# Performance work log

Measured on AMD Instinct MI355X. Metric: run time of the kernel, lower is better.

## Reference

```python
import jax, jax.numpy as jnp
import numpy as np

EPS = 1e-6
N_HEADS = 16
KV_HEADS = 4
HEAD_DIM = 64
N_REP = N_HEADS // KV_HEADS
N_EXPERTS = 8
TOP_K = 2


def _rms_norm(x, w):
    return x * jax.lax.rsqrt(jnp.mean(x * x, axis=-1, keepdims=True) + EPS) * w


def _apply_rope(x, fc):
    # x: (B,T,H,D); fc: (T, D//2, 2) holding (cos, sin)
    B, T, H, D = x.shape
    xr = x.reshape(B, T, H, D // 2, 2)
    f = fc.reshape(1, T, 1, D // 2, 2)
    re = xr[..., 0] * f[..., 0] - xr[..., 1] * f[..., 1]
    im = xr[..., 1] * f[..., 0] + xr[..., 0] * f[..., 1]
    return jnp.stack([re, im], axis=-1).reshape(B, T, H, D)


def _silu(x):
    return x * jax.nn.sigmoid(x)


def setup_inputs():
    key = jax.random.key(0)
    ks = jax.random.split(key, 16)
    B, T, C = 4, 1024, 1024
    IE, IS = 1024, 2048  # expert_inter_dim, shared inter_dim
    s = 0.02
    x = jax.random.normal(ks[0], (B, T, C), jnp.float32)
    inv_freq = 1.0 / (10000.0 ** (np.arange(0, HEAD_DIM, 2, dtype=np.float32) / HEAD_DIM))
    ang = np.outer(np.arange(T, dtype=np.float32), inv_freq)
    freq_cis = jnp.asarray(np.stack([np.cos(ang), np.sin(ang)], axis=-1), jnp.float32)
    causal = np.tril(np.ones((T, T), dtype=bool))
    mask = jnp.asarray(np.where(causal, 0.0, -1e9), dtype=jnp.float32).reshape(1, 1, T, T)
    window = jnp.zeros((1, 1, T, T), jnp.float32)
    return {
        "x": x,
        "freq_cis": freq_cis,
        "mask": mask,
        "window": window,
        "norm1_w": jnp.ones((C,), jnp.float32),
        "wq": jax.random.normal(ks[1], (N_HEADS * HEAD_DIM, C), jnp.float32) * s,
        "wk": jax.random.normal(ks[2], (KV_HEADS * HEAD_DIM, C), jnp.float32) * s,
        "wv": jax.random.normal(ks[3], (KV_HEADS * HEAD_DIM, C), jnp.float32) * s,
        "wo": jax.random.normal(ks[4], (C, N_HEADS * HEAD_DIM), jnp.float32) * s,
        "norm2_w": jnp.ones((C,), jnp.float32),
        "gate_w": jax.random.normal(ks[5], (N_EXPERTS, C), jnp.float32) * s,
        "exp_w1": jax.random.normal(ks[6], (N_EXPERTS, IE, C), jnp.float32) * s,
        "exp_w2": jax.random.normal(ks[7], (N_EXPERTS, IE, C), jnp.float32) * s,
        "exp_wp": jax.random.normal(ks[8], (N_EXPERTS, C, IE), jnp.float32) * s,
        "sh_w1": jax.random.normal(ks[9], (IS, C), jnp.float32) * s,
        "sh_w2": jax.random.normal(ks[10], (IS, C), jnp.float32) * s,
        "sh_wp": jax.random.normal(ks[11], (C, IS), jnp.float32) * s,
        "start_pos": 0,
    }


def reference(x, freq_cis, mask, window, norm1_w, wq, wk, wv, wo, norm2_w,
              gate_w, exp_w1, exp_w2, exp_wp, sh_w1, sh_w2, sh_wp, start_pos):
    B, T, C = x.shape
    # ---- pre-norm attention (GQA, Global mask, eval: no dropout) ----
    xn = _rms_norm(x, norm1_w)
    q = (xn @ wq.T).reshape(B, T, N_HEADS, HEAD_DIM)
    k = (xn @ wk.T).reshape(B, T, KV_HEADS, HEAD_DIM)
    v = (xn @ wv.T).reshape(B, T, KV_HEADS, HEAD_DIM)
    q = _apply_rope(q, freq_cis)
    k = _apply_rope(k, freq_cis)
    k = jnp.repeat(k, N_REP, axis=2)  # (B,T,H,D)
    v = jnp.repeat(v, N_REP, axis=2)
    scale = 1.0 / np.sqrt(HEAD_DIM).astype(np.float32)
    att = jnp.einsum("bqhd,bkhd->bhqk", q, k) * scale + mask
    p = jax.nn.softmax(att, axis=-1)
    o = jnp.einsum("bhqk,bkhd->bqhd", p, v).reshape(B, T, C)
    x = x + o @ wo.T
    # ---- pre-norm MoE FFN ----
    xn2 = _rms_norm(x, norm2_w).reshape(-1, C)  # (N,C)
    scores = xn2 @ gate_w.T                      # gate logits, returned
    probs = jax.nn.softmax(scores, axis=-1)
    top_w, top_i = jax.lax.top_k(probs, TOP_K)   # (N,K)
    # dense combine weights (N,E): zero for non-selected experts
    wfull = jnp.sum(jax.nn.one_hot(top_i, N_EXPERTS, dtype=x.dtype) * top_w[..., None], axis=1)
    h = _silu(jnp.einsum("nc,eic->eni", xn2, exp_w1)) * jnp.einsum("nc,eic->eni", xn2, exp_w2)
    ye = jnp.einsum("eni,eci->enc", h, exp_wp)   # per-expert outputs
    y = jnp.einsum("ne,enc->nc", wfull, ye)      # routed combine
    z = (_silu(xn2 @ sh_w1.T) * (xn2 @ sh_w2.T)) @ sh_wp.T  # shared expert
    out = x + (y + z).reshape(B, T, C)
    return out, scores
```

## Files before the change

kernel.cpp:

```cpp
#include <hip/hip_runtime.h>


typedef __bf16 bf16_t;
typedef __bf16 bf16x8 __attribute__((ext_vector_type(8)));
typedef __bf16 bf16x4 __attribute__((ext_vector_type(4)));
typedef float  f32x4  __attribute__((ext_vector_type(4)));

#define GLD16(gp, lp) __builtin_amdgcn_global_load_lds(                         \
    (const __attribute__((address_space(1))) void*)(gp),                        \
    (__attribute__((address_space(3))) void*)(lp), 16, 0, 0)

__global__ __launch_bounds__(256) void convert_k(
    const float* __restrict__ src, bf16_t* __restrict__ dst)
{
    size_t i = (size_t)blockIdx.x * 256 + threadIdx.x;
    float4 v = *((const float4*)src + i);
    bf16x4 o;
    o[0] = (bf16_t)v.x; o[1] = (bf16_t)v.y; o[2] = (bf16_t)v.z; o[3] = (bf16_t)v.w;
    *((bf16x4*)dst + i) = o;
}

__global__ __launch_bounds__(256) void gemm_bt(
    const bf16_t* __restrict__ A, const bf16_t* __restrict__ W,
    int M, int N, int K, int ldw, int mode,
    float* __restrict__ outF, bf16_t* __restrict__ outB,
    const float* __restrict__ resF)
{
    __shared__ __align__(16) bf16_t sA[128 * 64];
    __shared__ __align__(16) bf16_t sB[128 * 64];
    const int tid  = threadIdx.x;
    const int bm   = blockIdx.y * 128, bn = blockIdx.x * 128;
    const int lane = tid & 63;
    const int wv   = tid >> 6;
    const int wm   = (wv >> 1) * 64, wn = (wv & 1) * 64;
    const int lr   = lane & 15;
    const int kg   = lane >> 4;

    f32x4 acc[4][4];
    #pragma unroll
    for (int i = 0; i < 4; ++i)
        #pragma unroll
        for (int j = 0; j < 4; ++j)
            acc[i][j] = f32x4{0.f, 0.f, 0.f, 0.f};

    for (int k0 = 0; k0 < K; k0 += 64) {
        #pragma unroll
        for (int p = 0; p < 4; ++p) {
            int idx = p * 256 + tid;
            int row = idx >> 3, ch = (idx & 7) * 8;
            GLD16(A + (size_t)(bm + row) * K   + k0 + ch, sA + idx * 8);
            GLD16(W + (size_t)(bn + row) * ldw + k0 + ch, sB + idx * 8);
        }
        __syncthreads();
        #pragma unroll
        for (int ks = 0; ks < 2; ++ks) {
            bf16x8 af[4], bfr[4];
            #pragma unroll
            for (int i = 0; i < 4; ++i)
                af[i] = *(const bf16x8*)(sA + (wm + i * 16 + lr) * 64 + ks * 32 + kg * 8);
            #pragma unroll
            for (int j = 0; j < 4; ++j)
                bfr[j] = *(const bf16x8*)(sB + (wn + j * 16 + lr) * 64 + ks * 32 + kg * 8);
            #pragma unroll
            for (int i = 0; i < 4; ++i)
                #pragma unroll
                for (int j = 0; j < 4; ++j)
                    acc[i][j] = __builtin_amdgcn_mfma_f32_16x16x32_bf16(
                        af[i], bfr[j], acc[i][j], 0, 0, 0);
        }
        __syncthreads();
    }

    #pragma unroll
    for (int i = 0; i < 4; ++i) {
        #pragma unroll
        for (int j = 0; j < 4; ++j) {
            #pragma unroll
            for (int rr = 0; rr < 4; ++rr) {
                int m = bm + wm + i * 16 + kg * 4 + rr;
                int n = bn + wn + j * 16 + lr;
                size_t o = (size_t)m * N + n;
                float v = acc[i][j][rr];
                if (mode == 0)      outF[o] = v;
                else if (mode == 1) outB[o] = (bf16_t)v;
                else                outF[o] = v + resF[o];
            }
        }
    }
}

__global__ __launch_bounds__(256) void gemm_glu(
    const bf16_t* __restrict__ A, const bf16_t* __restrict__ W1,
    const bf16_t* __restrict__ W2, int M, int N, int K,
    bf16_t* __restrict__ out)
{
    __shared__ __align__(16) bf16_t sA[128 * 64];
    __shared__ __align__(16) bf16_t sB1[128 * 64];
    __shared__ __align__(16) bf16_t sB2[128 * 64];
    const int tid  = threadIdx.x;
    const int bm   = blockIdx.y * 128, bn = blockIdx.x * 128;
    const int lane = tid & 63;
    const int wv   = tid >> 6;
    const int wm   = (wv >> 1) * 64, wn = (wv & 1) * 64;
    const int lr   = lane & 15;
    const int kg   = lane >> 4;

    f32x4 acc1[4][4], acc2[4][4];
    #pragma unroll
    for (int i = 0; i < 4; ++i)
        #pragma unroll
        for (int j = 0; j < 4; ++j) {
            acc1[i][j] = f32x4{0.f, 0.f, 0.f, 0.f};
            acc2[i][j] = f32x4{0.f, 0.f, 0.f, 0.f};
        }

    for (int k0 = 0; k0 < K; k0 += 64) {
        #pragma unroll
        for (int p = 0; p < 4; ++p) {
            int idx = p * 256 + tid;
            int row = idx >> 3, ch = (idx & 7) * 8;
            GLD16(A  + (size_t)(bm + row) * K + k0 + ch, sA  + idx * 8);
            GLD16(W1 + (size_t)(bn + row) * K + k0 + ch, sB1 + idx * 8);
            GLD16(W2 + (size_t)(bn + row) * K + k0 + ch, sB2 + idx * 8);
        }
        __syncthreads();
        #pragma unroll
        for (int ks = 0; ks < 2; ++ks) {
            bf16x8 af[4], b1[4], b2[4];
            #pragma unroll
            for (int i = 0; i < 4; ++i)
                af[i] = *(const bf16x8*)(sA + (wm + i * 16 + lr) * 64 + ks * 32 + kg * 8);
            #pragma unroll
            for (int j = 0; j < 4; ++j) {
                b1[j] = *(const bf16x8*)(sB1 + (wn + j * 16 + lr) * 64 + ks * 32 + kg * 8);
                b2[j] = *(const bf16x8*)(sB2 + (wn + j * 16 + lr) * 64 + ks * 32 + kg * 8);
            }
            #pragma unroll
            for (int i = 0; i < 4; ++i)
                #pragma unroll
                for (int j = 0; j < 4; ++j) {
                    acc1[i][j] = __builtin_amdgcn_mfma_f32_16x16x32_bf16(
                        af[i], b1[j], acc1[i][j], 0, 0, 0);
                    acc2[i][j] = __builtin_amdgcn_mfma_f32_16x16x32_bf16(
                        af[i], b2[j], acc2[i][j], 0, 0, 0);
                }
        }
        __syncthreads();
    }

    #pragma unroll
    for (int i = 0; i < 4; ++i) {
        #pragma unroll
        for (int j = 0; j < 4; ++j) {
            #pragma unroll
            for (int rr = 0; rr < 4; ++rr) {
                int m = bm + wm + i * 16 + kg * 4 + rr;
                int n = bn + wn + j * 16 + lr;
                float v1 = acc1[i][j][rr], v2 = acc2[i][j][rr];
                out[(size_t)m * N + n] = (bf16_t)(v1 / (1.f + __expf(-v1)) * v2);
            }
        }
    }
}

__global__ __launch_bounds__(256) void glu_gather(
    const bf16_t* __restrict__ A, const bf16_t* __restrict__ W1,
    const bf16_t* __restrict__ W2, const int* __restrict__ tok_list,
    const int* __restrict__ cnt, const int* __restrict__ off,
    bf16_t* __restrict__ h)
{
    const int e = blockIdx.y >> 5, t = blockIdx.y & 31;
    const int ce = cnt[e];
    if (t * 128 >= ce) return;
    const int hbase = off[e] + t * 128;
    const bf16_t* W1e = W1 + (size_t)e * 1048576;
    const bf16_t* W2e = W2 + (size_t)e * 1048576;

    __shared__ __align__(16) bf16_t sA[128 * 64];
    __shared__ __align__(16) bf16_t sB1[128 * 64];
    __shared__ __align__(16) bf16_t sB2[128 * 64];
    const int tid  = threadIdx.x;
    const int bn   = blockIdx.x * 128;
    const int lane = tid & 63;
    const int wv   = tid >> 6;
    const int wm   = (wv >> 1) * 64, wn = (wv & 1) * 64;
    const int lr   = lane & 15;
    const int kg   = lane >> 4;

    int tok4[4];
    #pragma unroll
    for (int p = 0; p < 4; ++p)
        tok4[p] = tok_list[e * 4096 + t * 128 + p * 32 + (tid >> 3)];

    f32x4 acc1[4][4], acc2[4][4];
    #pragma unroll
    for (int i = 0; i < 4; ++i)
        #pragma unroll
        for (int j = 0; j < 4; ++j) {
            acc1[i][j] = f32x4{0.f, 0.f, 0.f, 0.f};
            acc2[i][j] = f32x4{0.f, 0.f, 0.f, 0.f};
        }

    for (int k0 = 0; k0 < 1024; k0 += 64) {
        #pragma unroll
        for (int p = 0; p < 4; ++p) {
            int idx = p * 256 + tid;
            int row = idx >> 3, ch = (idx & 7) * 8;
            GLD16(A   + (size_t)tok4[p] * 1024 + k0 + ch, sA  + idx * 8);
            GLD16(W1e + (size_t)(bn + row) * 1024 + k0 + ch, sB1 + idx * 8);
            GLD16(W2e + (size_t)(bn + row) * 1024 + k0 + ch, sB2 + idx * 8);
        }
        __syncthreads();
        #pragma unroll
        for (int ks = 0; ks < 2; ++ks) {
            bf16x8 af[4], b1[4], b2[4];
            #pragma unroll
            for (int i = 0; i < 4; ++i)
                af[i] = *(const bf16x8*)(sA + (wm + i * 16 + lr) * 64 + ks * 32 + kg * 8);
            #pragma unroll
            for (int j = 0; j < 4; ++j) {
                b1[j] = *(const bf16x8*)(sB1 + (wn + j * 16 + lr) * 64 + ks * 32 + kg * 8);
                b2[j] = *(const bf16x8*)(sB2 + (wn + j * 16 + lr) * 64 + ks * 32 + kg * 8);
            }
            #pragma unroll
            for (int i = 0; i < 4; ++i)
                #pragma unroll
                for (int j = 0; j < 4; ++j) {
                    acc1[i][j] = __builtin_amdgcn_mfma_f32_16x16x32_bf16(
                        af[i], b1[j], acc1[i][j], 0, 0, 0);
                    acc2[i][j] = __builtin_amdgcn_mfma_f32_16x16x32_bf16(
                        af[i], b2[j], acc2[i][j], 0, 0, 0);
                }
        }
        __syncthreads();
    }

    #pragma unroll
    for (int i = 0; i < 4; ++i) {
        #pragma unroll
        for (int j = 0; j < 4; ++j) {
            #pragma unroll
            for (int rr = 0; rr < 4; ++rr) {
                int rl = wm + i * 16 + kg * 4 + rr;
                int n  = bn + wn + j * 16 + lr;
                float v1 = acc1[i][j][rr], v2 = acc2[i][j][rr];
                h[(size_t)(hbase + rl) * 1024 + n] =
                    (bf16_t)(v1 / (1.f + __expf(-v1)) * v2);
            }
        }
    }
}

__global__ __launch_bounds__(256) void down_gather(
    const bf16_t* __restrict__ h, const bf16_t* __restrict__ Wp,
    const int* __restrict__ tok_list, const float* __restrict__ w_list,
    const int* __restrict__ cnt, const int* __restrict__ off,
    float* __restrict__ y)
{
    const int e = blockIdx.y >> 5, t = blockIdx.y & 31;
    const int ce = cnt[e];
    if (t * 128 >= ce) return;
    const int hbase = off[e] + t * 128;
    const bf16_t* We = Wp + (size_t)e * 1048576;

    __shared__ __align__(16) bf16_t sA[128 * 64];
    __shared__ __align__(16) bf16_t sB[128 * 64];
    const int tid  = threadIdx.x;
    const int bn   = blockIdx.x * 128;
    const int lane = tid & 63;
    const int wv   = tid >> 6;
    const int wm   = (wv >> 1) * 64, wn = (wv & 1) * 64;
    const int lr   = lane & 15;
    const int kg   = lane >> 4;

    f32x4 acc[4][4];
    #pragma unroll
    for (int i = 0; i < 4; ++i)
        #pragma unroll
        for (int j = 0; j < 4; ++j)
            acc[i][j] = f32x4{0.f, 0.f, 0.f, 0.f};

    for (int k0 = 0; k0 < 1024; k0 += 64) {
        #pragma unroll
        for (int p = 0; p < 4; ++p) {
            int idx = p * 256 + tid;
            int row = idx >> 3, ch = (idx & 7) * 8;
            GLD16(h  + (size_t)(hbase + row) * 1024 + k0 + ch, sA + idx * 8);
            GLD16(We + (size_t)(bn + row) * 1024 + k0 + ch,    sB + idx * 8);
        }
        __syncthreads();
        #pragma unroll
        for (int ks = 0; ks < 2; ++ks) {
            bf16x8 af[4], bfr[4];
            #pragma unroll
            for (int i = 0; i < 4; ++i)
                af[i] = *(const bf16x8*)(sA + (wm + i * 16 + lr) * 64 + ks * 32 + kg * 8);
            #pragma unroll
            for (int j = 0; j < 4; ++j)
                bfr[j] = *(const bf16x8*)(sB + (wn + j * 16 + lr) * 64 + ks * 32 + kg * 8);
            #pragma unroll
            for (int i = 0; i < 4; ++i)
                #pragma unroll
                for (int j = 0; j < 4; ++j)
                    acc[i][j] = __builtin_amdgcn_mfma_f32_16x16x32_bf16(
                        af[i], bfr[j], acc[i][j], 0, 0, 0);
        }
        __syncthreads();
    }

    #pragma unroll
    for (int i = 0; i < 4; ++i) {
        #pragma unroll
        for (int rr = 0; rr < 4; ++rr) {
            int rl = t * 128 + wm + i * 16 + kg * 4 + rr;
            if (rl < ce) {
                int   tok = tok_list[e * 4096 + rl];
                float wgt = w_list[e * 4096 + rl];
                #pragma unroll
                for (int j = 0; j < 4; ++j) {
                    int n = bn + wn + j * 16 + lr;
                    atomicAdd(&y[(size_t)tok * 1024 + n], wgt * acc[i][j][rr]);
                }
            }
        }
    }
}

__global__ __launch_bounds__(256) void rmsnorm_k(
    const float* __restrict__ src, const float* __restrict__ w,
    bf16_t* __restrict__ dst)
{
    const int row = blockIdx.x, tid = threadIdx.x;
    float4 t4 = *((const float4*)src + (size_t)row * 256 + tid);
    float ssum = t4.x*t4.x + t4.y*t4.y + t4.z*t4.z + t4.w*t4.w;
    #pragma unroll
    for (int off = 32; off > 0; off >>= 1) ssum += __shfl_down(ssum, off);
    __shared__ float red[4];
    if ((tid & 63) == 0) red[tid >> 6] = ssum;
    __syncthreads();
    float total = red[0] + red[1] + red[2] + red[3];
    float rms = rsqrtf(total * (1.0f / 1024.0f) + 1e-6f);
    float4 w4 = *((const float4*)w + tid);
    bf16x4 o4;
    o4[0] = (bf16_t)(t4.x * rms * w4.x);
    o4[1] = (bf16_t)(t4.y * rms * w4.y);
    o4[2] = (bf16_t)(t4.z * rms * w4.z);
    o4[3] = (bf16_t)(t4.w * rms * w4.w);
    *((bf16x4*)dst + (size_t)row * 256 + tid) = o4;
}

__global__ __launch_bounds__(256) void rmsnorm_gate_k(
    const float* __restrict__ src, const float* __restrict__ w,
    const float* __restrict__ gw, bf16_t* __restrict__ dst,
    float* __restrict__ scores, int* __restrict__ topi,
    float* __restrict__ topw)
{
    const int row = blockIdx.x, tid = threadIdx.x;
    float4 t4 = *((const float4*)src + (size_t)row * 256 + tid);
    float ssum = t4.x*t4.x + t4.y*t4.y + t4.z*t4.z + t4.w*t4.w;
    #pragma unroll
    for (int off = 32; off > 0; off >>= 1) ssum += __shfl_down(ssum, off);
    __shared__ float red[4];
    if ((tid & 63) == 0) red[tid >> 6] = ssum;
    __syncthreads();
    float total = red[0] + red[1] + red[2] + red[3];
    float rms = rsqrtf(total * (1.0f / 1024.0f) + 1e-6f);
    float4 w4 = *((const float4*)w + tid);
    float4 f4;
    f4.x = t4.x * rms * w4.x;
    f4.y = t4.y * rms * w4.y;
    f4.z = t4.z * rms * w4.z;
    f4.w = t4.w * rms * w4.w;
    bf16x4 o4;
    o4[0] = (bf16_t)f4.x; o4[1] = (bf16_t)f4.y;
    o4[2] = (bf16_t)f4.z; o4[3] = (bf16_t)f4.w;
    *((bf16x4*)dst + (size_t)row * 256 + tid) = o4;

    float a[8];
    #pragma unroll
    for (int e = 0; e < 8; ++e) {
        float4 g4 = *((const float4*)(gw + (size_t)e * 1024) + tid);
        a[e] = f4.x * g4.x + f4.y * g4.y + f4.z * g4.z + f4.w * g4.w;
    }
    #pragma unroll
    for (int e = 0; e < 8; ++e)
        #pragma unroll
        for (int off = 32; off > 0; off >>= 1) a[e] += __shfl_down(a[e], off);
    __shared__ float gred[4][8];
    if ((tid & 63) == 0)
        #pragma unroll
        for (int e = 0; e < 8; ++e) gred[tid >> 6][e] = a[e];
    __syncthreads();
    if (tid == 0) {
        float lg[8];
        #pragma unroll
        for (int e = 0; e < 8; ++e)
            lg[e] = gred[0][e] + gred[1][e] + gred[2][e] + gred[3][e];
        #pragma unroll
        for (int e = 0; e < 8; ++e) scores[(size_t)row * 8 + e] = lg[e];
        float mx = lg[0];
        #pragma unroll
        for (int e = 1; e < 8; ++e) mx = fmaxf(mx, lg[e]);
        float p[8], sum = 0.f;
        #pragma unroll
        for (int e = 0; e < 8; ++e) { p[e] = __expf(lg[e] - mx); sum += p[e]; }
        float inv = 1.0f / sum;
        #pragma unroll
        for (int e = 0; e < 8; ++e) p[e] *= inv;
        int i1 = 0;
        #pragma unroll
        for (int e = 1; e < 8; ++e) if (p[e] > p[i1]) i1 = e;
        int i2 = (i1 == 0) ? 1 : 0;
        #pragma unroll
        for (int e = 0; e < 8; ++e) if (e != i1 && p[e] > p[i2]) i2 = e;
        topi[row] = i1 | (i2 << 8);
        topw[row * 2]     = p[i1];
        topw[row * 2 + 1] = p[i2];
    }
}

__global__ __launch_bounds__(256) void build_lists_k(
    const int* __restrict__ topi, const float* __restrict__ topw,
    int* __restrict__ tok_list, float* __restrict__ w_list,
    int* __restrict__ cnt)
{
    const int e = blockIdx.x;
    const int tid = threadIdx.x, lane = tid & 63, wv = tid >> 6;
    __shared__ int wc[4];
    int base = 0;
    for (int t0 = 0; t0 < 4096; t0 += 256) {
        int tok = t0 + tid;
        int ti = topi[tok];
        int i1 = ti & 255, i2 = (ti >> 8) & 255;
        bool m = (i1 == e) || (i2 == e);
        unsigned long long b = __ballot(m);
        if (lane == 0) wc[wv] = __popcll(b);
        __syncthreads();
        int pos = base;
        #pragma unroll
        for (int k = 0; k < 4; ++k) if (k < wv) pos += wc[k];
        pos += __popcll(b & ((1ull << lane) - 1ull));
        if (m) {
            tok_list[e * 4096 + pos] = tok;
            w_list[e * 4096 + pos]   = (i1 == e) ? topw[tok * 2] : topw[tok * 2 + 1];
        }
        base += wc[0] + wc[1] + wc[2] + wc[3];
        __syncthreads();
    }
    int padded = (base + 127) & ~127;
    for (int p = base + tid; p < padded; p += 256) tok_list[e * 4096 + p] = 0;
    if (tid == 0) cnt[e] = base;
}

__global__ void plan_k(const int* __restrict__ cnt, int* __restrict__ off)
{
    if (threadIdx.x == 0) {
        int run = 0;
        for (int e = 0; e < 8; ++e) {
            off[e] = run;
            run += (cnt[e] + 127) & ~127;
        }
    }
}

__global__ __launch_bounds__(256) void rope_k(
    bf16_t* __restrict__ buf, const float* __restrict__ fc, int nh)
{
    int idx = blockIdx.x * 256 + threadIdx.x;
    int pr = idx & 31;
    int hn = idx >> 5;
    int h  = hn % nh;
    int n  = hn / nh;
    int tpos = n & 1023;
    const float* f = fc + ((size_t)tpos * 32 + pr) * 2;
    float c = f[0], s = f[1];
    size_t base = ((size_t)n * nh + h) * 64 + pr * 2;
    float x0 = (float)buf[base], x1 = (float)buf[base + 1];
    buf[base]     = (bf16_t)(x0 * c - x1 * s);
    buf[base + 1] = (bf16_t)(x1 * c + x0 * s);
}

__global__ __launch_bounds__(256) void transpose_v(
    const bf16_t* __restrict__ vb, bf16_t* __restrict__ vt)
{
    __shared__ bf16_t tile[64][72];
    const int tt = blockIdx.x, kvh = blockIdx.y, b = blockIdx.z;
    const int tid = threadIdx.x;
    {
        int r = tid >> 2, c = (tid & 3) * 16;
        const bf16_t* src = vb + ((size_t)(b * 1024 + tt * 64 + r)) * 256 + kvh * 64 + c;
        bf16x8 v0 = *(const bf16x8*)src;
        bf16x8 v1 = *(const bf16x8*)(src + 8);
        *(bf16x8*)&tile[r][c] = v0;
        *(bf16x8*)&tile[r][c + 8] = v1;
    }
    __syncthreads();
    {
        int d = tid >> 2, t4 = (tid & 3) * 16;
        bf16_t* dst = vt + ((size_t)((b * 4 + kvh) * 64 + d)) * 1024 + tt * 64 + t4;
        bf16x8 o0, o1;
        #pragma unroll
        for (int u = 0; u < 8; ++u) {
            o0[u] = tile[t4 + u][d];
            o1[u] = tile[t4 + 8 + u][d];
        }
        *(bf16x8*)dst = o0;
        *(bf16x8*)(dst + 8) = o1;
    }
}

__global__ __launch_bounds__(256) void attn_mfma(
    const bf16_t* __restrict__ qb, const bf16_t* __restrict__ kb,
    const bf16_t* __restrict__ vt, bf16_t* __restrict__ ob)
{
    const int qt = blockIdx.x, h = blockIdx.y, b = blockIdx.z;
    const int kvh = h >> 2;
    __shared__ __align__(16) bf16_t sK[64 * 64];
    __shared__ __align__(16) bf16_t sVt[64 * 64];
    __shared__ __align__(16) bf16_t sP[64 * 72];
    const int tid  = threadIdx.x;
    const int w    = tid >> 6;
    const int lane = tid & 63;
    const int lr   = lane & 15;
    const int kg   = lane >> 4;

    bf16x8 qf[2];
    {
        const bf16_t* qrow = qb + ((size_t)(b * 1024 + qt * 64 + w * 16 + lr)) * 1024 + h * 64;
        qf[0] = *(const bf16x8*)(qrow + kg * 8);
        qf[1] = *(const bf16x8*)(qrow + 32 + kg * 8);
    }
    float m_run[4], l_run[4];
    f32x4 o_acc[4];
    #pragma unroll
    for (int rr = 0; rr < 4; ++rr) { m_run[rr] = -1.0e30f; l_run[rr] = 0.f; }
    #pragma unroll
    for (int dt = 0; dt < 4; ++dt) o_acc[dt] = f32x4{0.f, 0.f, 0.f, 0.f};

    for (int kt = 0; kt <= qt; ++kt) {
        #pragma unroll
        for (int p = 0; p < 2; ++p) {
            int idx = p * 256 + tid;
            int row = idx >> 3, ch = (idx & 7) * 8;
            GLD16(kb + ((size_t)(b * 1024 + kt * 64 + row)) * 256 + kvh * 64 + ch,
                  sK + idx * 8);
            GLD16(vt + ((size_t)((b * 4 + kvh) * 64 + row)) * 1024 + kt * 64 + ch,
                  sVt + idx * 8);
        }
        __syncthreads();

        f32x4 sfr[4];
        #pragma unroll
        for (int j = 0; j < 4; ++j) {
            sfr[j] = f32x4{0.f, 0.f, 0.f, 0.f};
            #pragma unroll
            for (int ks = 0; ks < 2; ++ks) {
                bf16x8 bf = *(const bf16x8*)(sK + (j * 16 + lr) * 64 + ks * 32 + kg * 8);
                sfr[j] = __builtin_amdgcn_mfma_f32_16x16x32_bf16(qf[ks], bf, sfr[j], 0, 0, 0);
            }
        }
        const int rowg = qt * 64 + w * 16 + kg * 4;
        float mnew[4];
        #pragma unroll
        for (int rr = 0; rr < 4; ++rr) mnew[rr] = m_run[rr];
        #pragma unroll
        for (int j = 0; j < 4; ++j) {
            int colg = kt * 64 + j * 16 + lr;
            #pragma unroll
            for (int rr = 0; rr < 4; ++rr) {
                float s = sfr[j][rr] * 0.125f;
                if (colg > rowg + rr) s = -1.0e30f;
                sfr[j][rr] = s;
                mnew[rr] = fmaxf(mnew[rr], s);
            }
        }
        #pragma unroll
        for (int off = 1; off < 16; off <<= 1)
            #pragma unroll
            for (int rr = 0; rr < 4; ++rr)
                mnew[rr] = fmaxf(mnew[rr], __shfl_xor(mnew[rr], off, 64));
        float alpha[4], lpart[4];
        #pragma unroll
        for (int rr = 0; rr < 4; ++rr) {
            alpha[rr] = __expf(m_run[rr] - mnew[rr]);
            lpart[rr] = 0.f;
        }
        #pragma unroll
        for (int j = 0; j < 4; ++j)
            #pragma unroll
            for (int rr = 0; rr < 4; ++rr) {
                float p = __expf(sfr[j][rr] - mnew[rr]);
                sfr[j][rr] = p;
                lpart[rr] += p;
            }
        #pragma unroll
        for (int j = 0; j < 4; ++j)
            #pragma unroll
            for (int rr = 0; rr < 4; ++rr)
                sP[(w * 16 + kg * 4 + rr) * 72 + j * 16 + lr] = (bf16_t)sfr[j][rr];
        #pragma unroll
        for (int off = 1; off < 16; off <<= 1)
            #pragma unroll
            for (int rr = 0; rr < 4; ++rr)
                lpart[rr] += __shfl_xor(lpart[rr], off, 64);
        #pragma unroll
        for (int rr = 0; rr < 4; ++rr) {
            l_run[rr] = l_run[rr] * alpha[rr] + lpart[rr];
            m_run[rr] = mnew[rr];
        }
        #pragma unroll
        for (int dt = 0; dt < 4; ++dt)
            #pragma unroll
            for (int rr = 0; rr < 4; ++rr)
                o_acc[dt][rr] *= alpha[rr];
        #pragma unroll
        for (int ks = 0; ks < 2; ++ks) {
            bf16x8 af = *(const bf16x8*)(sP + (w * 16 + lr) * 72 + ks * 32 + kg * 8);
            #pragma unroll
            for (int dt = 0; dt < 4; ++dt) {
                bf16x8 bf = *(const bf16x8*)(sVt + (dt * 16 + lr) * 64 + ks * 32 + kg * 8);
                o_acc[dt] = __builtin_amdgcn_mfma_f32_16x16x32_bf16(af, bf, o_acc[dt], 0, 0, 0);
            }
        }
        __syncthreads();
    }

    float inv[4];
    #pragma unroll
    for (int rr = 0; rr < 4; ++rr) inv[rr] = 1.0f / l_run[rr];
    #pragma unroll
    for (int dt = 0; dt < 4; ++dt)
        #pragma unroll
        for (int rr = 0; rr < 4; ++rr) {
            int tok = qt * 64 + w * 16 + kg * 4 + rr;
            ob[((size_t)(b * 1024 + tok)) * 1024 + h * 64 + dt * 16 + lr] =
                (bf16_t)(o_acc[dt][rr] * inv[rr]);
        }
}

__global__ __launch_bounds__(256) void finalize_k(
    const float* __restrict__ x1, const float* __restrict__ y, float* __restrict__ out)
{
    size_t i = (size_t)blockIdx.x * 256 + threadIdx.x;
    float4 a = *((const float4*)x1 + i);
    float4 b = *((const float4*)y + i);
    float4 o4;
    o4.x = a.x + b.x; o4.y = a.y + b.y; o4.z = a.z + b.z; o4.w = a.w + b.w;
    *((float4*)out + i) = o4;
}

extern "C" void kernel_launch(void* const* d_in, const int* in_sizes, int n_in,
                              void* d_out, int out_size, void* d_ws, size_t ws_size,
                              hipStream_t stream)
{
    const float* x   = (const float*)d_in[0];
    const float* fc  = (const float*)d_in[1];
    const float* n1w = (const float*)d_in[4];
    const float* wq  = (const float*)d_in[5];
    const float* wk  = (const float*)d_in[6];
    const float* wv  = (const float*)d_in[7];
    const float* wo  = (const float*)d_in[8];
    const float* n2w = (const float*)d_in[9];
    const float* gw  = (const float*)d_in[10];
    const float* ew1 = (const float*)d_in[11];
    const float* ew2 = (const float*)d_in[12];
    const float* ewp = (const float*)d_in[13];
    const float* sw1 = (const float*)d_in[14];
    const float* sw2 = (const float*)d_in[15];
    const float* swp = (const float*)d_in[16];

    const size_t MB = 1024 * 1024;
    char* ws = (char*)d_ws;
    bf16_t* xnb  = (bf16_t*)(ws + 0);
    float*  x1   = (float*) (ws + 8 * MB);
    float*  y    = (float*) (ws + 24 * MB);
    char*   slotA= ws + 40 * MB;
    bf16_t* h    = (bf16_t*)(ws + 56 * MB);
    char*   lists= ws + 74 * MB;
    int*    tok_list = (int*)lists;
    float*  w_list   = (float*)(lists + 131072);
    int*    cnt      = (int*)(lists + 262144);
    int*    off      = (int*)(lists + 262208);
    int*    topi     = (int*)(lists + 262400);
    float*  topw     = (float*)(lists + 278784);
    bf16_t* qb   = (bf16_t*)(ws + 75 * MB);
    bf16_t* kb   = (bf16_t*)(ws + 83 * MB);
    bf16_t* vb   = (bf16_t*)(ws + 85 * MB);
    bf16_t* ob   = (bf16_t*)(ws + 87 * MB);
    bf16_t* vt   = (bf16_t*)(ws + 95 * MB);

    float* outp   = (float*)d_out;
    float* scores = outp + (size_t)4096 * 1024;

    auto conv = [&](const float* s, bf16_t* d, size_t cntN) {
        convert_k<<<cntN / 1024, 256, 0, stream>>>(s, d);
    };
    auto gemm = [&](const bf16_t* A, const bf16_t* W, int M, int N, int K, int ldw,
                    int mode, float* oF, bf16_t* oB, const float* res) {
        gemm_bt<<<dim3(N / 128, M / 128), 256, 0, stream>>>(
            A, W, M, N, K, ldw, mode, oF, oB, res);
    };
    auto glu = [&](const bf16_t* A, const bf16_t* W1, const bf16_t* W2,
                   int M, int N, int K, bf16_t* o) {
        gemm_glu<<<dim3(N / 128, M / 128), 256, 0, stream>>>(A, W1, W2, M, N, K, o);
    };

    bf16_t* wqb = (bf16_t*)slotA;
    bf16_t* wkb = wqb + 1048576;
    bf16_t* wvb = wkb + 262144;
    bf16_t* wob = wvb + 262144;
    conv(wq, wqb, 1048576);
    conv(wk, wkb, 262144);
    conv(wv, wvb, 262144);
    conv(wo, wob, 1048576);

    rmsnorm_k<<<4096, 256, 0, stream>>>(x, n1w, xnb);
    gemm(xnb, wqb, 4096, 1024, 1024, 1024, 1, nullptr, qb, nullptr);
    gemm(xnb, wkb, 4096, 256, 1024, 1024, 1, nullptr, kb, nullptr);
    gemm(xnb, wvb, 4096, 256, 1024, 1024, 1, nullptr, vb, nullptr);
    rope_k<<<(4096 * 16 * 32) / 256, 256, 0, stream>>>(qb, fc, 16);
    rope_k<<<(4096 * 4 * 32) / 256, 256, 0, stream>>>(kb, fc, 4);
    transpose_v<<<dim3(16, 4, 4), 256, 0, stream>>>(vb, vt);
    attn_mfma<<<dim3(16, 16, 4), 256, 0, stream>>>(qb, kb, vt, ob);
    gemm(ob, wob, 4096, 1024, 1024, 1024, 2, x1, nullptr, x);

    rmsnorm_gate_k<<<4096, 256, 0, stream>>>(x1, n2w, gw, xnb, scores, topi, topw);
    build_lists_k<<<8, 256, 0, stream>>>(topi, topw, tok_list, w_list, cnt);
    plan_k<<<1, 64, 0, stream>>>(cnt, off);

    bf16_t* sw1b = (bf16_t*)(ws + 75 * MB);
    bf16_t* sw2b = sw1b + 2097152;
    bf16_t* swpb = sw2b + 2097152;
    conv(sw1, sw1b, 2097152);
    conv(sw2, sw2b, 2097152);
    conv(swp, swpb, 2097152);
    bf16_t* hb = (bf16_t*)slotA;
    glu(xnb, sw1b, sw2b, 4096, 2048, 1024, hb);
    gemm(hb, swpb, 4096, 1024, 2048, 2048, 0, y, nullptr, nullptr);

    bf16_t* ew1b = (bf16_t*)slotA;
    bf16_t* ew2b = (bf16_t*)(ws + 75 * MB);
    conv(ew1, ew1b, 8388608);
    conv(ew2, ew2b, 8388608);
    glu_gather<<<dim3(8, 256), 256, 0, stream>>>(xnb, ew1b, ew2b,
                                                 tok_list, cnt, off, h);
    bf16_t* ewpb = (bf16_t*)slotA;
    conv(ewp, ewpb, 8388608);
    down_gather<<<dim3(8, 256), 256, 0, stream>>>(h, ewpb,
                                                  tok_list, w_list, cnt, off, y);

    finalize_k<<<(4096 * 1024) / 1024, 256, 0, stream>>>(x1, y, outp);
    (void)in_sizes; (void)n_in; (void)out_size; (void)ws_size;
}
```

Measured before the change: 740.7 us.

## Merge shared and routed expert GEMMs into grouped launches, swizzle attention LDS

The shared-expert GLU and the routed-expert gather GLU now run in one grouped kernel, and the two down projections share a second grouped kernel that atomically accumulates straight into the output. The output is pre-seeded with the attention residual by the wo GEMM epilogue, which removes the y buffer, its separate write and the finalize pass, and fills the GPU better by overlapping the shared and routed work. Separately, the K and V^T tiles in attention use an XOR swizzle on LDS columns to cut bank conflicts. The cost is that the shared-expert results also go through atomics, and the workspace buffers are reshuffled to fit the weight copies side by side, which risks aliasing.

```diff
diff --git a/kernel.cpp b/kernel.cpp
--- a/kernel.cpp
+++ b/kernel.cpp
@@ -24,7 +24,7 @@
     const bf16_t* __restrict__ A, const bf16_t* __restrict__ W,
     int M, int N, int K, int ldw, int mode,
     float* __restrict__ outF, bf16_t* __restrict__ outB,
-    const float* __restrict__ resF)
+    const float* __restrict__ resF, float* __restrict__ outF2)
 {
     __shared__ __align__(16) bf16_t sA[128 * 64];
     __shared__ __align__(16) bf16_t sB[128 * 64];
@@ -83,28 +83,59 @@
                 float v = acc[i][j][rr];
                 if (mode == 0)      outF[o] = v;
                 else if (mode == 1) outB[o] = (bf16_t)v;
-                else                outF[o] = v + resF[o];
-            }
-        }
-    }
-}
-
-__global__ __launch_bounds__(256) void gemm_glu(
-    const bf16_t* __restrict__ A, const bf16_t* __restrict__ W1,
-    const bf16_t* __restrict__ W2, int M, int N, int K,
-    bf16_t* __restrict__ out)
-{
+                else {
+                    float r = v + resF[o];
+                    outF[o] = r;
+                    if (outF2) outF2[o] = r;
+                }
+            }
+        }
+    }
+}
+
+__global__ __launch_bounds__(256) void glu_merged(
+    const bf16_t* __restrict__ A, const bf16_t* __restrict__ eW1,
+    const bf16_t* __restrict__ eW2, const bf16_t* __restrict__ sW1,
+    const bf16_t* __restrict__ sW2, const int* __restrict__ tok_list,
+    const int* __restrict__ cnt, const int* __restrict__ off,
+    bf16_t* __restrict__ h_r, bf16_t* __restrict__ h_s)
+{
+    const int ybl = blockIdx.y;
+    const int bn  = blockIdx.x * 128;
+    const int tid = threadIdx.x;
+
+    int t, hbase, ldh, ebase = 0;
+    const bf16_t *W1, *W2;
+    bf16_t* hout;
+    bool sj = (ybl < 32);
+    if (sj) {
+        t = ybl; hbase = t * 128; ldh = 2048;
+        W1 = sW1; W2 = sW2; hout = h_s;
+    } else {
+        int e = (ybl - 32) >> 5; t = (ybl - 32) & 31;
+        if (bn >= 1024) return;
+        if (t * 128 >= cnt[e]) return;
+        hbase = off[e] + t * 128; ldh = 1024;
+        W1 = eW1 + (size_t)e * 1048576; W2 = eW2 + (size_t)e * 1048576;
+        hout = h_r; ebase = e * 4096;
+    }
+
     __shared__ __align__(16) bf16_t sA[128 * 64];
     __shared__ __align__(16) bf16_t sB1[128 * 64];
     __shared__ __align__(16) bf16_t sB2[128 * 64];
-    const int tid  = threadIdx.x;
-    const int bm   = blockIdx.y * 128, bn = blockIdx.x * 128;
     const int lane = tid & 63;
     const int wv   = tid >> 6;
     const int wm   = (wv >> 1) * 64, wn = (wv & 1) * 64;
     const int lr   = lane & 15;
     const int kg   = lane >> 4;
 
+    int tok4[4];
+    #pragma unroll
+    for (int p = 0; p < 4; ++p) {
+        int rowp = (p * 256 + tid) >> 3;
+        tok4[p] = sj ? (t * 128 + rowp) : tok_list[ebase + t * 128 + rowp];
+    }
+
     f32x4 acc1[4][4], acc2[4][4];
     #pragma unroll
     for (int i = 0; i < 4; ++i)
@@ -114,14 +145,14 @@
             acc2[i][j] = f32x4{0.f, 0.f, 0.f, 0.f};
         }
 
-    for (int k0 = 0; k0 < K; k0 += 64) {
+    for (int k0 = 0; k0 < 1024; k0 += 64) {
         #pragma unroll
         for (int p = 0; p < 4; ++p) {
             int idx = p * 256 + tid;
             int row = idx >> 3, ch = (idx & 7) * 8;
-            GLD16(A  + (size_t)(bm + row) * K + k0 + ch, sA  + idx * 8);
-            GLD16(W1 + (size_t)(bn + row) * K + k0 + ch, sB1 + idx * 8);
-            GLD16(W2 + (size_t)(bn + row) * K + k0 + ch, sB2 + idx * 8);
+            GLD16(A  + (size_t)tok4[p] * 1024 + k0 + ch,     sA  + idx * 8);
+            GLD16(W1 + (size_t)(bn + row) * 1024 + k0 + ch,  sB1 + idx * 8);
+            GLD16(W2 + (size_t)(bn + row) * 1024 + k0 + ch,  sB2 + idx * 8);
         }
         __syncthreads();
         #pragma unroll
@@ -154,139 +185,66 @@
         for (int j = 0; j < 4; ++j) {
             #pragma unroll
             for (int rr = 0; rr < 4; ++rr) {
-                int m = bm + wm + i * 16 + kg * 4 + rr;
-                int n = bn + wn + j * 16 + lr;
+                int rl = wm + i * 16 + kg * 4 + rr;
+                int n  = bn + wn + j * 16 + lr;
                 float v1 = acc1[i][j][rr], v2 = acc2[i][j][rr];
-                out[(size_t)m * N + n] = (bf16_t)(v1 / (1.f + __expf(-v1)) * v2);
-            }
-        }
-    }
-}
-
-__global__ __launch_bounds__(256) void glu_gather(
-    const bf16_t* __restrict__ A, const bf16_t* __restrict__ W1,
-    const bf16_t* __restrict__ W2, const int* __restrict__ tok_list,
+                hout[(size_t)(hbase + rl) * ldh + n] =
+                    (bf16_t)(v1 / (1.f + __expf(-v1)) * v2);
+            }
+        }
+    }
+}
+
+__global__ __launch_bounds__(256) void down_merged(
+    const bf16_t* __restrict__ h_r, const bf16_t* __restrict__ h_s,
+    const bf16_t* __restrict__ eWp, const bf16_t* __restrict__ sWp,
+    const int* __restrict__ tok_list, const float* __restrict__ w_list,
     const int* __restrict__ cnt, const int* __restrict__ off,
-    bf16_t* __restrict__ h)
-{
-    const int e = blockIdx.y >> 5, t = blockIdx.y & 31;
-    const int ce = cnt[e];
-    if (t * 128 >= ce) return;
-    const int hbase = off[e] + t * 128;
-    const bf16_t* W1e = W1 + (size_t)e * 1048576;
-    const bf16_t* W2e = W2 + (size_t)e * 1048576;
+    float* __restrict__ out)
+{
+    const int ybl = blockIdx.y;
+    const int bn  = blockIdx.x * 128;
+    const int tid = threadIdx.x;
+
+    int t, KK, ce = 0, ebase = 0;
+    const bf16_t *Ab, *W;
+    bool sj = (ybl < 32);
+    if (sj) {
+        t = ybl; KK = 2048;
+        Ab = h_s + (size_t)(t * 128) * 2048;
+        W  = sWp;
+    } else {
+        int e = (ybl - 32) >> 5; t = (ybl - 32) & 31;
+        ce = cnt[e];
+        if (t * 128 >= ce) return;
+        KK = 1024;
+        Ab = h_r + (size_t)(off[e] + t * 128) * 1024;
+        W  = eWp + (size_t)e * 1048576;
+        ebase = e * 4096;
+    }
 
     __shared__ __align__(16) bf16_t sA[128 * 64];
-    __shared__ __align__(16) bf16_t sB1[128 * 64];
-    __shared__ __align__(16) bf16_t sB2[128 * 64];
-    const int tid  = threadIdx.x;
-    const int bn   = blockIdx.x * 128;
+    __shared__ __align__(16) bf16_t sB[128 * 64];
     const int lane = tid & 63;
     const int wv   = tid >> 6;
     const int wm   = (wv >> 1) * 64, wn = (wv & 1) * 64;
     const int lr   = lane & 15;
     const int kg   = lane >> 4;
 
-    int tok4[4];
-    #pragma unroll
-    for (int p = 0; p < 4; ++p)
-        tok4[p] = tok_list[e * 4096 + t * 128 + p * 32 + (tid >> 3)];
-
-    f32x4 acc1[4][4], acc2[4][4];
+    f32x4 acc[4][4];
     #pragma unroll
     for (int i = 0; i < 4; ++i)
         #pragma unroll
-        for (int j = 0; j < 4; ++j) {
-            acc1[i][j] = f32x4{0.f, 0.f, 0.f, 0.f};
-            acc2[i][j] = f32x4{0.f, 0.f, 0.f, 0.f};
-        }
-
-    for (int k0 = 0; k0 < 1024; k0 += 64) {
+        for (int j = 0; j < 4; ++j)
+            acc[i][j] = f32x4{0.f, 0.f, 0.f, 0.f};
+
+    for (int k0 = 0; k0 < KK; k0 += 64) {
         #pragma unroll
         for (int p = 0; p < 4; ++p) {
             int idx = p * 256 + tid;
             int row = idx >> 3, ch = (idx & 7) * 8;
-            GLD16(A   + (size_t)tok4[p] * 1024 + k0 + ch, sA  + idx * 8);
-            GLD16(W1e + (size_t)(bn + row) * 1024 + k0 + ch, sB1 + idx * 8);
-            GLD16(W2e + (size_t)(bn + row) * 1024 + k0 + ch, sB2 + idx * 8);
-        }
-        __syncthreads();
-        #pragma unroll
-        for (int ks = 0; ks < 2; ++ks) {
-            bf16x8 af[4], b1[4], b2[4];
-            #pragma unroll
-            for (int i = 0; i < 4; ++i)
-                af[i] = *(const bf16x8*)(sA + (wm + i * 16 + lr) * 64 + ks * 32 + kg * 8);
-            #pragma unroll
-            for (int j = 0; j < 4; ++j) {
-                b1[j] = *(const bf16x8*)(sB1 + (wn + j * 16 + lr) * 64 + ks * 32 + kg * 8);
-                b2[j] = *(const bf16x8*)(sB2 + (wn + j * 16 + lr) * 64 + ks * 32 + kg * 8);
-            }
-            #pragma unroll
-            for (int i = 0; i < 4; ++i)
-                #pragma unroll
-                for (int j = 0; j < 4; ++j) {
-                    acc1[i][j] = __builtin_amdgcn_mfma_f32_16x16x32_bf16(
-                        af[i], b1[j], acc1[i][j], 0, 0, 0);
-                    acc2[i][j] = __builtin_amdgcn_mfma_f32_16x16x32_bf16(
-                        af[i], b2[j], acc2[i][j], 0, 0, 0);
-                }
-        }
-        __syncthreads();
-    }
-
-    #pragma unroll
-    for (int i = 0; i < 4; ++i) {
-        #pragma unroll
-        for (int j = 0; j < 4; ++j) {
-            #pragma unroll
-            for (int rr = 0; rr < 4; ++rr) {
-                int rl = wm + i * 16 + kg * 4 + rr;
-                int n  = bn + wn + j * 16 + lr;
-                float v1 = acc1[i][j][rr], v2 = acc2[i][j][rr];
-                h[(size_t)(hbase + rl) * 1024 + n] =
-                    (bf16_t)(v1 / (1.f + __expf(-v1)) * v2);
-            }
-        }
-    }
-}
-
-__global__ __launch_bounds__(256) void down_gather(
-    const bf16_t* __restrict__ h, const bf16_t* __restrict__ Wp,
-    const int* __restrict__ tok_list, const float* __restrict__ w_list,
-    const int* __restrict__ cnt, const int* __restrict__ off,
-    float* __restrict__ y)
-{
-    const int e = blockIdx.y >> 5, t = blockIdx.y & 31;
-    const int ce = cnt[e];
-    if (t * 128 >= ce) return;
-    const int hbase = off[e] + t * 128;
-    const bf16_t* We = Wp + (size_t)e * 1048576;
-
-    __shared__ __align__(16) bf16_t sA[128 * 64];
-    __shared__ __align__(16) bf16_t sB[128 * 64];
-    const int tid  = threadIdx.x;
-    const int bn   = blockIdx.x * 128;
-    const int lane = tid & 63;
-    const int wv   = tid >> 6;
-    const int wm   = (wv >> 1) * 64, wn = (wv & 1) * 64;
-    const int lr   = lane & 15;
-    const int kg   = lane >> 4;
-
-    f32x4 acc[4][4];
-    #pragma unroll
-    for (int i = 0; i < 4; ++i)
-        #pragma unroll
-        for (int j = 0; j < 4; ++j)
-            acc[i][j] = f32x4{0.f, 0.f, 0.f, 0.f};
-
-    for (int k0 = 0; k0 < 1024; k0 += 64) {
-        #pragma unroll
-        for (int p = 0; p < 4; ++p) {
-            int idx = p * 256 + tid;
-            int row = idx >> 3, ch = (idx & 7) * 8;
-            GLD16(h  + (size_t)(hbase + row) * 1024 + k0 + ch, sA + idx * 8);
-            GLD16(We + (size_t)(bn + row) * 1024 + k0 + ch,    sB + idx * 8);
+            GLD16(Ab + (size_t)row * KK + k0 + ch,         sA + idx * 8);
+            GLD16(W  + (size_t)(bn + row) * KK + k0 + ch,  sB + idx * 8);
         }
         __syncthreads();
         #pragma unroll
@@ -312,14 +270,21 @@
     for (int i = 0; i < 4; ++i) {
         #pragma unroll
         for (int rr = 0; rr < 4; ++rr) {
-            int rl = t * 128 + wm + i * 16 + kg * 4 + rr;
-            if (rl < ce) {
-                int   tok = tok_list[e * 4096 + rl];
-                float wgt = w_list[e * 4096 + rl];
+            int rl = wm + i * 16 + kg * 4 + rr;
+            int tok; float wgt; bool valid;
+            if (sj) {
+                tok = t * 128 + rl; wgt = 1.0f; valid = true;
+            } else {
+                int g = t * 128 + rl;
+                valid = (g < ce);
+                tok = valid ? tok_list[ebase + g] : 0;
+                wgt = valid ? w_list[ebase + g] : 0.f;
+            }
+            if (valid) {
                 #pragma unroll
                 for (int j = 0; j < 4; ++j) {
                     int n = bn + wn + j * 16 + lr;
-                    atomicAdd(&y[(size_t)tok * 1024 + n], wgt * acc[i][j][rr]);
+                    atomicAdd(&out[(size_t)tok * 1024 + n], wgt * acc[i][j][rr]);
                 }
             }
         }
@@ -523,6 +488,7 @@
     const int lane = tid & 63;
     const int lr   = lane & 15;
     const int kg   = lane >> 4;
+    const int swz  = (lr & 7) << 3;
 
     bf16x8 qf[2];
     {
@@ -541,10 +507,11 @@
         #pragma unroll
         for (int p = 0; p < 2; ++p) {
             int idx = p * 256 + tid;
-            int row = idx >> 3, ch = (idx & 7) * 8;
-            GLD16(kb + ((size_t)(b * 1024 + kt * 64 + row)) * 256 + kvh * 64 + ch,
+            int row = idx >> 3;
+            int chs = ((idx & 7) * 8) ^ ((row & 7) << 3);
+            GLD16(kb + ((size_t)(b * 1024 + kt * 64 + row)) * 256 + kvh * 64 + chs,
                   sK + idx * 8);
-            GLD16(vt + ((size_t)((b * 4 + kvh) * 64 + row)) * 1024 + kt * 64 + ch,
+            GLD16(vt + ((size_t)((b * 4 + kvh) * 64 + row)) * 1024 + kt * 64 + chs,
                   sVt + idx * 8);
         }
         __syncthreads();
@@ -555,7 +522,8 @@
             sfr[j] = f32x4{0.f, 0.f, 0.f, 0.f};
             #pragma unroll
             for (int ks = 0; ks < 2; ++ks) {
-                bf16x8 bf = *(const bf16x8*)(sK + (j * 16 + lr) * 64 + ks * 32 + kg * 8);
+                bf16x8 bf = *(const bf16x8*)(sK + (j * 16 + lr) * 64 +
+                                             ((ks * 32 + kg * 8) ^ swz));
                 sfr[j] = __builtin_amdgcn_mfma_f32_16x16x32_bf16(qf[ks], bf, sfr[j], 0, 0, 0);
             }
         }
@@ -618,7 +586,8 @@
             bf16x8 af = *(const bf16x8*)(sP + (w * 16 + lr) * 72 + ks * 32 + kg * 8);
             #pragma unroll
             for (int dt = 0; dt < 4; ++dt) {
-                bf16x8 bf = *(const bf16x8*)(sVt + (dt * 16 + lr) * 64 + ks * 32 + kg * 8);
+                bf16x8 bf = *(const bf16x8*)(sVt + (dt * 16 + lr) * 64 +
+                                             ((ks * 32 + kg * 8) ^ swz));
                 o_acc[dt] = __builtin_amdgcn_mfma_f32_16x16x32_bf16(af, bf, o_acc[dt], 0, 0, 0);
             }
         }
@@ -636,17 +605,6 @@
             ob[((size_t)(b * 1024 + tok)) * 1024 + h * 64 + dt * 16 + lr] =
                 (bf16_t)(o_acc[dt][rr] * inv[rr]);
         }
-}
-
-__global__ __launch_bounds__(256) void finalize_k(
-    const float* __restrict__ x1, const float* __restrict__ y, float* __restrict__ out)
-{
-    size_t i = (size_t)blockIdx.x * 256 + threadIdx.x;
-    float4 a = *((const float4*)x1 + i);
-    float4 b = *((const float4*)y + i);
-    float4 o4;
-    o4.x = a.x + b.x; o4.y = a.y + b.y; o4.z = a.z + b.z; o4.w = a.w + b.w;
-    *((float4*)out + i) = o4;
 }
 
 extern "C" void kernel_launch(void* const* d_in, const int* in_sizes, int n_in,
@@ -673,8 +631,12 @@
     char* ws = (char*)d_ws;
     bf16_t* xnb  = (bf16_t*)(ws + 0);
     float*  x1   = (float*) (ws + 8 * MB);
-    float*  y    = (float*) (ws + 24 * MB);
+    bf16_t* ew2b = (bf16_t*)(ws + 8 * MB);
+    bf16_t* sw1b = (bf16_t*)(ws + 24 * MB);
+    bf16_t* sw2b = (bf16_t*)(ws + 28 * MB);
+    bf16_t* swpb = (bf16_t*)(ws + 32 * MB);
     char*   slotA= ws + 40 * MB;
+    bf16_t* hb   = (bf16_t*)slotA;
     bf16_t* h    = (bf16_t*)(ws + 56 * MB);
     char*   lists= ws + 74 * MB;
     int*    tok_list = (int*)lists;
@@ -688,6 +650,8 @@
     bf16_t* vb   = (bf16_t*)(ws + 85 * MB);
     bf16_t* ob   = (bf16_t*)(ws + 87 * MB);
     bf16_t* vt   = (bf16_t*)(ws + 95 * MB);
+    bf16_t* ew1b = (bf16_t*)(ws + 75 * MB);
+    bf16_t* ewpb = (bf16_t*)(ws + 75 * MB);
 
     float* outp   = (float*)d_out;
     float* scores = outp + (size_t)4096 * 1024;
@@ -696,13 +660,9 @@
         convert_k<<<cntN / 1024, 256, 0, stream>>>(s, d);
     };
     auto gemm = [&](const bf16_t* A, const bf16_t* W, int M, int N, int K, int ldw,
-                    int mode, float* oF, bf16_t* oB, const float* res) {
+                    int mode, float* oF, bf16_t* oB, const float* res, float* oF2) {
         gemm_bt<<<dim3(N / 128, M / 128), 256, 0, stream>>>(
-            A, W, M, N, K, ldw, mode, oF, oB, res);
-    };
-    auto glu = [&](const bf16_t* A, const bf16_t* W1, const bf16_t* W2,
-                   int M, int N, int K, bf16_t* o) {
-        gemm_glu<<<dim3(N / 128, M / 128), 256, 0, stream>>>(A, W1, W2, M, N, K, o);
+            A, W, M, N, K, ldw, mode, oF, oB, res, oF2);
     };
 
     bf16_t* wqb = (bf16_t*)slotA;
@@ -713,42 +673,34 @@
     conv(wk, wkb, 262144);
     conv(wv, wvb, 262144);
     conv(wo, wob, 1048576);
+    conv(sw1, sw1b, 2097152);
+    conv(sw2, sw2b, 2097152);
+    conv(swp, swpb, 2097152);
 
     rmsnorm_k<<<4096, 256, 0, stream>>>(x, n1w, xnb);
-    gemm(xnb, wqb, 4096, 1024, 1024, 1024, 1, nullptr, qb, nullptr);
-    gemm(xnb, wkb, 4096, 256, 1024, 1024, 1, nullptr, kb, nullptr);
-    gemm(xnb, wvb, 4096, 256, 1024, 1024, 1, nullptr, vb, nullptr);
+    gemm(xnb, wqb, 4096, 1024, 1024, 1024, 1, nullptr, qb, nullptr, nullptr);
+    gemm(xnb, wkb, 4096, 256, 1024, 1024, 1, nullptr, kb, nullptr, nullptr);
+    gemm(xnb, wvb, 4096, 256, 1024, 1024, 1, nullptr, vb, nullptr, nullptr);
     rope_k<<<(4096 * 16 * 32) / 256, 256, 0, stream>>>(qb, fc, 16);
     rope_k<<<(4096 * 4 * 32) / 256, 256, 0, stream>>>(kb, fc, 4);
     transpose_v<<<dim3(16, 4, 4), 256, 0, stream>>>(vb, vt);
     attn_mfma<<<dim3(16, 16, 4), 256, 0, stream>>>(qb, kb, vt, ob);
-    gemm(ob, wob, 4096, 1024, 1024, 1024, 2, x1, nullptr, x);
+    gemm(ob, wob, 4096, 1024, 1024, 1024, 2, x1, nullptr, x, outp);
 
     rmsnorm_gate_k<<<4096, 256, 0, stream>>>(x1, n2w, gw, xnb, scores, topi, topw);
     build_lists_k<<<8, 256, 0, stream>>>(topi, topw, tok_list, w_list, cnt);
     plan_k<<<1, 64, 0, stream>>>(cnt, off);
 
-    bf16_t* sw1b = (bf16_t*)(ws + 75 * MB);
-    bf16_t* sw2b = sw1b + 2097152;
-    bf16_t* swpb = sw2b + 2097152;
-    conv(sw1, sw1b, 2097152);
-    conv(sw2, sw2b, 2097152);
-    conv(swp, swpb, 2097152);
-    bf16_t* hb = (bf16_t*)slotA;
-    glu(xnb, sw1b, sw2b, 4096, 2048, 1024, hb);
-    gemm(hb, swpb, 4096, 1024, 2048, 2048, 0, y, nullptr, nullptr);
-
-    bf16_t* ew1b = (bf16_t*)slotA;
-    bf16_t* ew2b = (bf16_t*)(ws + 75 * MB);
     conv(ew1, ew1b, 8388608);
     conv(ew2, ew2b, 8388608);
-    glu_gather<<<dim3(8, 256), 256, 0, stream>>>(xnb, ew1b, ew2b,
-                                                 tok_list, cnt, off, h);
-    bf16_t* ewpb = (bf16_t*)slotA;
+
+    glu_merged<<<dim3(16, 288), 256, 0, stream>>>(
+        xnb, ew1b, ew2b, sw1b, sw2b, tok_list, cnt, off, h, hb);
+
     conv(ewp, ewpb, 8388608);
-    down_gather<<<dim3(8, 256), 256, 0, stream>>>(h, ewpb,
-                                                  tok_list, w_list, cnt, off, y);
-
-    finalize_k<<<(4096 * 1024) / 1024, 256, 0, stream>>>(x1, y, outp);
+
+    down_merged<<<dim3(8, 288), 256, 0, stream>>>(
+        h, hb, ewpb, swpb, tok_list, w_list, cnt, off, outp);
+
     (void)in_sizes; (void)n_in; (void)out_size; (void)ws_size;
 }
```

Result: no change. 749.7 us (+1.2%).
